# Performance work log

Hardware: AMD Instinct MI355X
Metric: run time of the kernel (lower is better)

Reference implementation:

```python
import jax, jax.numpy as jnp
from jax import lax
import numpy as np

P_NUM = 63
CHANNEL = 64
KSIZE = 5
PAD = KSIZE // 2
MEAN = jnp.linspace(-310.0, 310.0, P_NUM).reshape(1, 1, P_NUM, 1, 1)
DN = ('NCHW', 'OIHW', 'NCHW')


def rep_pad(x, p=PAD):
    return jnp.pad(x, ((0, 0), (0, 0), (p, p), (p, p)), mode='edge')


def conv(x, w, b):
    out = lax.conv_general_dilated(x, w, (1, 1), 'VALID', dimension_numbers=DN)
    return out + b[None, :, None, None]


def conv_transpose(x, w):
    # torch conv_transpose2d with weight (in, out, k, k), stride 1, no pad ==
    # full correlation with spatially flipped, in/out-transposed kernel
    k = jnp.flip(w, (-2, -1)).transpose(1, 0, 2, 3)  # (out, in, k, k)
    kh = KSIZE - 1
    return lax.conv_general_dilated(x, k, (1, 1), [(kh, kh), (kh, kh)], dimension_numbers=DN)


def crop(x, p=PAD):
    return x[:, :, p:-p, p:-p]


def act(x, w, gradient=False):
    # x: (B,C,H,W); w: (1,C,P,1,1); Gaussian-mixture RBF activation
    d = x[:, :, None, :, :] - MEAN                 # (B,C,P,H,W)
    g = jnp.exp(d * d / -200.0)
    if gradient:
        g = g * (d / -100.0)
    return (g * w).sum(axis=2)                     # (B,C,H,W)


def setup_inputs() -> dict:
    key = jax.random.key(0)
    ks = jax.random.split(key, 8)
    B, H, W = 4, 128, 128
    return {
        'x': jax.random.uniform(ks[0], (B, 1, H, W), jnp.float32),
        'y': jax.random.uniform(ks[1], (B, 1, H, W), jnp.float32),
        'lam': 0,
        'f0': jax.random.normal(ks[2], (CHANNEL, 1, KSIZE, KSIZE), jnp.float32) * 0.1,
        'b0': jax.random.normal(ks[3], (CHANNEL,), jnp.float32) * 0.01,
        'f1': jax.random.normal(ks[4], (1, CHANNEL, KSIZE, KSIZE), jnp.float32) * 0.1,
        'b1': jax.random.normal(ks[5], (1,), jnp.float32) * 0.01,
        'w0': jax.random.normal(ks[6], (1, CHANNEL, P_NUM, 1, 1), jnp.float32) * 0.1,
        'w1': jax.random.normal(ks[7], (1, 1, P_NUM, 1, 1), jnp.float32) * 0.1,
        'lam_param': jnp.float32(np.log(0.1)),
    }


def reference(x, y, lam, f0, b0, f1, b1, w0, w1, lam_param):
    del lam  # third forward arg is ignored by the original module
    x = x * 255.0
    y = y * 255.0
    xx = x
    # encoder
    c0 = conv(rep_pad(x), f0, b0)        # (B,C,H,W)
    a0 = act(c0, w0)
    c1 = conv(rep_pad(a0), f1, b1)       # (B,1,H,W)
    a1 = act(c1, w1)
    # decoder (gradient-like path)
    d = crop(conv_transpose(a1, f1))     # (B,C,H,W)
    d = d * act(c0, w0, gradient=True)
    d = crop(conv_transpose(d, f0))      # (B,1,H,W)
    out = (xx - (d + jnp.exp(lam_param) * (xx - y))) / 255.0
    return out
```

## Files before the change

kernel.cpp:

```cpp
#include <hip/hip_runtime.h>
#include <hip/hip_bf16.h>

#define BSZ 4
#define CH 64
#define IH 128
#define IW 128
#define PN 63
#define TLS 32
#define TLH 36
#define XSD 40
#define NT 64
#define CG 4
#define NG 16
#define NPOS 324
#define NPIX (BSZ*IH*IW)
#define BT 384
#define TBN 142
#define TBH 5.0f
#define TBLO (-355.0f)

__global__ __launch_bounds__(160) void kT(const float* __restrict__ w0,
                                          const float* __restrict__ w1,
                                          float4* __restrict__ tab) {
    __shared__ float wsh[PN];
    const int ch = blockIdx.x;
    const float* w = (ch < CH) ? (w0 + (size_t)ch * PN) : w1;
    if (threadIdx.x < PN) wsh[threadIdx.x] = w[threadIdx.x];
    __syncthreads();
    const int i = threadIdx.x;
    if (i >= TBN) return;
    const float x0 = TBLO + TBH * i, xm = x0 + 0.5f * TBH, x1 = x0 + TBH;
    float f0 = 0.f, fm = 0.f, f1 = 0.f;
    for (int p = 0; p < PN; ++p) {
        const float mu = -310.0f + 10.0f * (float)p, wv = wsh[p];
        const float d0 = x0 - mu, dm = xm - mu, d1 = x1 - mu;
        f0 = __fmaf_rn(wv, __expf(d0 * d0 * -0.005f), f0);
        fm = __fmaf_rn(wv, __expf(dm * dm * -0.005f), fm);
        f1 = __fmaf_rn(wv, __expf(d1 * d1 * -0.005f), f1);
    }
    tab[(size_t)ch * TBN + i] =
        make_float4(f0, -3.f * f0 + 4.f * fm - f1, 2.f * f0 - 4.f * fm + 2.f * f1, 0.f);
}

__device__ __forceinline__ void act_tab4(const float* __restrict__ v,
                                         const float4* __restrict__ tb,
                                         float* __restrict__ av,
                                         float* __restrict__ ag) {
    float t[4];
    int idx[4];
#pragma unroll
    for (int k = 0; k < 4; ++k) {
        float u = __fmaf_rn(v[k], 1.0f / TBH, -TBLO / TBH);
        u = fminf(fmaxf(u, 0.0f), (float)TBN);
        idx[k] = min((int)u, TBN - 1);
        t[k] = u - (float)idx[k];
    }
    float4 c[4];
#pragma unroll
    for (int k = 0; k < 4; ++k) c[k] = tb[idx[k]];
#pragma unroll
    for (int k = 0; k < 4; ++k) {
        av[k] = __fmaf_rn(t[k], __fmaf_rn(t[k], c[k].z, c[k].y), c[k].x);
        ag[k] = __fmaf_rn(t[k] + t[k], c[k].z, c[k].y) * (1.0f / TBH);
    }
}

__device__ __forceinline__ float act_tab_v(float v, const float4* __restrict__ tb) {
    float u = __fmaf_rn(v, 1.0f / TBH, -TBLO / TBH);
    u = fminf(fmaxf(u, 0.0f), (float)TBN);
    const int idx = min((int)u, TBN - 1);
    const float t = u - (float)idx;
    const float4 c = tb[idx];
    return __fmaf_rn(t, __fmaf_rn(t, c.z, c.y), c.x);
}

__global__ __launch_bounds__(BT) void kAB(const float* __restrict__ x,
                                          const float* __restrict__ f0,
                                          const float* __restrict__ b0,
                                          const float* __restrict__ f1,
                                          const float4* __restrict__ tab,
                                          float* __restrict__ c1p,
                                          __hip_bfloat16* __restrict__ g0out) {
    __shared__ float xs[XSD * XSD];
    __shared__ float a0s[CG][TLH * TLH];
    __shared__ float4 tbs[CG][TBN];

    const int tile = blockIdx.x;
    const int cgi  = blockIdx.y;
    const int cg   = cgi * CG;
    const int b    = tile >> 4;
    const int t    = tile & 15;
    const int h0   = (t >> 2) * TLS;
    const int w0p  = (t & 3) * TLS;
    const int tid  = threadIdx.x;

    for (int i = tid; i < XSD * XSD; i += BT) {
        int iy = i / XSD, ix = i - iy * XSD;
        int gy = min(max(h0 + iy - 4, 0), IH - 1);
        int gx = min(max(w0p + ix - 4, 0), IW - 1);
        xs[i] = x[((size_t)b * IH + gy) * IW + gx] * 255.0f;
    }
    for (int i = tid; i < CG * TBN; i += BT) {
        int cc = i / TBN, k = i - cc * TBN;
        tbs[cc][k] = tab[(size_t)(cg + cc) * TBN + k];
    }
    __syncthreads();

    if (tid < NPOS) {
        const int p = tid;
        const int pyb = p / 18, pxb = p - pyb * 18;
        const int py = 2 * pyb, px = 2 * pxb;
        float win[6][6];
#pragma unroll
        for (int r = 0; r < 6; ++r) {
            const float2* rp = (const float2*)&xs[(py + r) * XSD + px];
            float2 p0 = rp[0], p1 = rp[1], p2 = rp[2];
            win[r][0] = p0.x; win[r][1] = p0.y; win[r][2] = p1.x;
            win[r][3] = p1.y; win[r][4] = p2.x; win[r][5] = p2.y;
        }
        const bool vint = (py >= 2) && (py < 34) && (px >= 2) && (px < 34);
        const int gy0 = h0 + py - 2, gx0 = w0p + px - 2;

#pragma unroll
        for (int cc = 0; cc < CG; ++cc) {
            const int c = cg + cc;
            const float bias = b0[c];
            float acc[4] = {bias, bias, bias, bias};
#pragma unroll
            for (int u = 0; u < 5; ++u)
#pragma unroll
                for (int v = 0; v < 5; ++v) {
                    const float kv = f0[(size_t)c * 25 + u * 5 + v];
                    acc[0] = __fmaf_rn(win[u][v],         kv, acc[0]);
                    acc[1] = __fmaf_rn(win[u][v + 1],     kv, acc[1]);
                    acc[2] = __fmaf_rn(win[u + 1][v],     kv, acc[2]);
                    acc[3] = __fmaf_rn(win[u + 1][v + 1], kv, acc[3]);
                }
            float av[4], ag[4];
            act_tab4(acc, tbs[cc], av, ag);
            *(float2*)&a0s[cc][py * TLH + px]       = make_float2(av[0], av[1]);
            *(float2*)&a0s[cc][(py + 1) * TLH + px] = make_float2(av[2], av[3]);
            if (vint) {
                const size_t gb = ((size_t)b * CH + c) * (IH * IW);
                __hip_bfloat162 r0 = {__float2bfloat16(ag[0]), __float2bfloat16(ag[1])};
                __hip_bfloat162 r1 = {__float2bfloat16(ag[2]), __float2bfloat16(ag[3])};
                *(__hip_bfloat162*)&g0out[gb + (size_t)gy0 * IW + gx0]       = r0;
                *(__hip_bfloat162*)&g0out[gb + (size_t)(gy0 + 1) * IW + gx0] = r1;
            }
        }
    }
    __syncthreads();

    if (h0 == 0 || h0 == IH - TLS || w0p == 0 || w0p == IW - TLS) {
        for (int p = tid; p < TLH * TLH; p += BT) {
            const int py = p / TLH, px = p - py * TLH;
            const int gy = h0 + py - 2, gx = w0p + px - 2;
            if ((unsigned)gy >= IH || (unsigned)gx >= IW) {
                const int cpy = min(max(gy, 0), IH - 1) - h0 + 2;
                const int cpx = min(max(gx, 0), IW - 1) - w0p + 2;
                const int src = cpy * TLH + cpx;
#pragma unroll
                for (int cc = 0; cc < CG; ++cc)
                    a0s[cc][p] = a0s[cc][src];
            }
        }
    }
    __syncthreads();

    if (tid < 256) {
        const int lx = tid & 15, ly = tid >> 4;
        const int r0 = 2 * ly, c0 = 2 * lx;
        float a00 = 0.f, a01 = 0.f, a10 = 0.f, a11 = 0.f;

#pragma unroll
        for (int cc = 0; cc < CG; ++cc) {
            float win[6][6];
#pragma unroll
            for (int r = 0; r < 6; ++r) {
                const float2* rp = (const float2*)&a0s[cc][(r0 + r) * TLH + c0];
                float2 p0 = rp[0], p1 = rp[1], p2 = rp[2];
                win[r][0] = p0.x; win[r][1] = p0.y; win[r][2] = p1.x;
                win[r][3] = p1.y; win[r][4] = p2.x; win[r][5] = p2.y;
            }
#pragma unroll
            for (int u = 0; u < 5; ++u)
#pragma unroll
                for (int v = 0; v < 5; ++v) {
                    const float kv = f1[(size_t)(cg + cc) * 25 + u * 5 + v];
                    a00 = __fmaf_rn(win[u][v],         kv, a00);
                    a01 = __fmaf_rn(win[u][v + 1],     kv, a01);
                    a10 = __fmaf_rn(win[u + 1][v],     kv, a10);
                    a11 = __fmaf_rn(win[u + 1][v + 1], kv, a11);
                }
        }

        const size_t base = (size_t)cgi * NPIX + ((size_t)b * IH + h0 + r0) * IW + w0p + c0;
        *(float2*)&c1p[base]      = make_float2(a00, a01);
        *(float2*)&c1p[base + IW] = make_float2(a10, a11);
    }
}

__global__ __launch_bounds__(256) void kB2(const float* __restrict__ c1p,
                                           const float* __restrict__ b1,
                                           const float4* __restrict__ tab,
                                           float* __restrict__ a1) {
    __shared__ float4 tbs[TBN];
    const int tid = threadIdx.x;
    if (tid < TBN) tbs[tid] = tab[(size_t)CH * TBN + tid];
    __syncthreads();

    const int pid = blockIdx.x * 256 + tid;
    float vv = b1[0];
#pragma unroll
    for (int g = 0; g < NG; ++g) vv += c1p[(size_t)g * NPIX + pid];
    a1[pid] = act_tab_v(vv, tbs);
}

__global__ __launch_bounds__(BT) void kCD(const float* __restrict__ a1,
                                          const float* __restrict__ f1,
                                          const float* __restrict__ f0,
                                          const __hip_bfloat16* __restrict__ g0,
                                          float* __restrict__ d3p) {
    __shared__ float a1s[XSD * XSD];
    __shared__ float dbs[CG][TLH * TLH];

    const int tile = blockIdx.x;
    const int cgi  = blockIdx.y;
    const int cg   = cgi * CG;
    const int b    = tile >> 4;
    const int t    = tile & 15;
    const int h0   = (t >> 2) * TLS;
    const int w0p  = (t & 3) * TLS;
    const int tid  = threadIdx.x;

    for (int p = tid; p < XSD * XSD; p += BT) {
        int iy = p / XSD, ix = p - iy * XSD;
        int gy = h0 + iy - 4, gx = w0p + ix - 4;
        float v = 0.0f;
        if ((unsigned)gy < IH && (unsigned)gx < IW)
            v = a1[((size_t)b * IH + gy) * IW + gx];
        a1s[p] = v;
    }
    __syncthreads();

    if (tid < NPOS) {
        const int p = tid;
        const int pyb = p / 18, pxb = p - pyb * 18;
        const int py = 2 * pyb, px = 2 * pxb;
        const int gy0 = h0 + py - 2, gx0 = w0p + px - 2;
        const bool inb = ((unsigned)gy0 < IH) && ((unsigned)gx0 < IW);

        __hip_bfloat162 gr0[CG], gr1[CG];
#pragma unroll
        for (int cc = 0; cc < CG; ++cc) {
            __hip_bfloat162 z; z.x = __float2bfloat16(0.f); z.y = z.x;
            gr0[cc] = z; gr1[cc] = z;
            if (inb) {
                const size_t gb = ((size_t)b * CH + cg + cc) * (IH * IW);
                gr0[cc] = *(const __hip_bfloat162*)&g0[gb + (size_t)gy0 * IW + gx0];
                gr1[cc] = *(const __hip_bfloat162*)&g0[gb + (size_t)(gy0 + 1) * IW + gx0];
            }
        }

        float win[6][6];
#pragma unroll
        for (int r = 0; r < 6; ++r) {
            const float2* rp = (const float2*)&a1s[(py + r) * XSD + px];
            float2 p0 = rp[0], p1 = rp[1], p2 = rp[2];
            win[r][0] = p0.x; win[r][1] = p0.y; win[r][2] = p1.x;
            win[r][3] = p1.y; win[r][4] = p2.x; win[r][5] = p2.y;
        }

#pragma unroll
        for (int cc = 0; cc < CG; ++cc) {
            const int c = cg + cc;
            float d00 = 0.f, d01 = 0.f, d10 = 0.f, d11 = 0.f;
#pragma unroll
            for (int u = 0; u < 5; ++u)
#pragma unroll
                for (int v = 0; v < 5; ++v) {
                    const float kv = f1[(size_t)c * 25 + u * 5 + v];
                    d00 = __fmaf_rn(win[4 - u][4 - v], kv, d00);
                    d01 = __fmaf_rn(win[4 - u][5 - v], kv, d01);
                    d10 = __fmaf_rn(win[5 - u][4 - v], kv, d10);
                    d11 = __fmaf_rn(win[5 - u][5 - v], kv, d11);
                }
            const float o00 = d00 * __bfloat162float(gr0[cc].x);
            const float o01 = d01 * __bfloat162float(gr0[cc].y);
            const float o10 = d10 * __bfloat162float(gr1[cc].x);
            const float o11 = d11 * __bfloat162float(gr1[cc].y);
            *(float2*)&dbs[cc][py * TLH + px]       = make_float2(o00, o01);
            *(float2*)&dbs[cc][(py + 1) * TLH + px] = make_float2(o10, o11);
        }
    }
    __syncthreads();

    if (tid < 256) {
        const int lx = tid & 15, ly = tid >> 4;
        const int r0 = 2 * ly, c0 = 2 * lx;
        float a00 = 0.f, a01 = 0.f, a10 = 0.f, a11 = 0.f;

#pragma unroll
        for (int cc = 0; cc < CG; ++cc) {
            float win[6][6];
#pragma unroll
            for (int r = 0; r < 6; ++r) {
                const float2* rp = (const float2*)&dbs[cc][(r0 + r) * TLH + c0];
                float2 p0 = rp[0], p1 = rp[1], p2 = rp[2];
                win[r][0] = p0.x; win[r][1] = p0.y; win[r][2] = p1.x;
                win[r][3] = p1.y; win[r][4] = p2.x; win[r][5] = p2.y;
            }
#pragma unroll
            for (int u = 0; u < 5; ++u)
#pragma unroll
                for (int v = 0; v < 5; ++v) {
                    const float kv = f0[(size_t)(cg + cc) * 25 + u * 5 + v];
                    a00 = __fmaf_rn(win[4 - u][4 - v], kv, a00);
                    a01 = __fmaf_rn(win[4 - u][5 - v], kv, a01);
                    a10 = __fmaf_rn(win[5 - u][4 - v], kv, a10);
                    a11 = __fmaf_rn(win[5 - u][5 - v], kv, a11);
                }
        }

        const size_t base = (size_t)cgi * NPIX + ((size_t)b * IH + h0 + r0) * IW + w0p + c0;
        *(float2*)&d3p[base]      = make_float2(a00, a01);
        *(float2*)&d3p[base + IW] = make_float2(a10, a11);
    }
}

__global__ __launch_bounds__(256) void kE(const float* __restrict__ d3p,
                                          const float* __restrict__ x,
                                          const float* __restrict__ y,
                                          const float* __restrict__ lam_param,
                                          float* __restrict__ out) {
    const int pid = blockIdx.x * 256 + threadIdx.x;
    float d3 = 0.0f;
#pragma unroll
    for (int g = 0; g < NG; ++g) d3 += d3p[(size_t)g * NPIX + pid];
    const float elam = __expf(lam_param[0]);
    const float xv = x[pid], yv = y[pid];
    out[pid] = xv - d3 * (1.0f / 255.0f) - elam * (xv - yv);
}

extern "C" void kernel_launch(void* const* d_in, const int* in_sizes, int n_in,
                              void* d_out, int out_size, void* d_ws, size_t ws_size,
                              hipStream_t stream) {
    const float* x   = (const float*)d_in[0];
    const float* y   = (const float*)d_in[1];
    const float* f0  = (const float*)d_in[3];
    const float* b0  = (const float*)d_in[4];
    const float* f1  = (const float*)d_in[5];
    const float* b1  = (const float*)d_in[6];
    const float* w0  = (const float*)d_in[7];
    const float* w1  = (const float*)d_in[8];
    const float* lam = (const float*)d_in[9];
    float* out = (float*)d_out;

    const size_t nch = (size_t)BSZ * CH * IH * IW;
    __hip_bfloat16* g0 = (__hip_bfloat16*)d_ws;
    float4* tab = (float4*)(g0 + nch);
    float* c1p  = (float*)(tab + (size_t)(CH + 1) * TBN);
    float* a1   = c1p + (size_t)NG * NPIX;
    float* d3p  = a1 + NPIX;

    kT <<<CH + 1, 160, 0, stream>>>(w0, w1, tab);
    kAB<<<dim3(NT, NG), BT, 0, stream>>>(x, f0, b0, f1, tab, c1p, g0);
    kB2<<<NPIX / 256, 256, 0, stream>>>(c1p, b1, tab, a1);
    kCD<<<dim3(NT, NG), BT, 0, stream>>>(a1, f1, f0, g0, d3p);
    kE <<<NPIX / 256, 256, 0, stream>>>(d3p, x, y, lam, out);
}
```

Baseline: 121.5 us.

## Fuse c1 partial reduction into kCD and store partials as bf16

Removes the kB2 kernel: kCD now sums the 16 channel-group partials of c1 for its halo tile and applies the w1 activation table on the fly. The c1 and d3 partial buffers are stored in bf16 instead of fp32, halving their write and read traffic. In exchange, each kCD block redoes the 16-way reduction and table lookup for its overlapping halo (and all 16 channel-group blocks repeat it), and bf16 partials lose precision in values scaled by 255.

```diff
diff --git a/kernel.cpp b/kernel.cpp
--- a/kernel.cpp
+++ b/kernel.cpp
@@ -65,7 +65,7 @@
     }
 }
 
-__device__ __forceinline__ float act_tab_v(float v, const float4* __restrict__ tb) {
+__device__ __forceinline__ float act_tab_g(float v, const float4* __restrict__ tb) {
     float u = __fmaf_rn(v, 1.0f / TBH, -TBLO / TBH);
     u = fminf(fmaxf(u, 0.0f), (float)TBN);
     const int idx = min((int)u, TBN - 1);
@@ -79,7 +79,7 @@
                                           const float* __restrict__ b0,
                                           const float* __restrict__ f1,
                                           const float4* __restrict__ tab,
-                                          float* __restrict__ c1p,
+                                          __hip_bfloat16* __restrict__ c1p,
                                           __hip_bfloat16* __restrict__ g0out) {
     __shared__ float xs[XSD * XSD];
     __shared__ float a0s[CG][TLH * TLH];
@@ -195,32 +195,20 @@
         }
 
         const size_t base = (size_t)cgi * NPIX + ((size_t)b * IH + h0 + r0) * IW + w0p + c0;
-        *(float2*)&c1p[base]      = make_float2(a00, a01);
-        *(float2*)&c1p[base + IW] = make_float2(a10, a11);
-    }
-}
-
-__global__ __launch_bounds__(256) void kB2(const float* __restrict__ c1p,
-                                           const float* __restrict__ b1,
-                                           const float4* __restrict__ tab,
-                                           float* __restrict__ a1) {
-    __shared__ float4 tbs[TBN];
-    const int tid = threadIdx.x;
-    if (tid < TBN) tbs[tid] = tab[(size_t)CH * TBN + tid];
-    __syncthreads();
-
-    const int pid = blockIdx.x * 256 + tid;
-    float vv = b1[0];
-#pragma unroll
-    for (int g = 0; g < NG; ++g) vv += c1p[(size_t)g * NPIX + pid];
-    a1[pid] = act_tab_v(vv, tbs);
-}
-
-__global__ __launch_bounds__(BT) void kCD(const float* __restrict__ a1,
+        __hip_bfloat162 q0 = {__float2bfloat16(a00), __float2bfloat16(a01)};
+        __hip_bfloat162 q1 = {__float2bfloat16(a10), __float2bfloat16(a11)};
+        *(__hip_bfloat162*)&c1p[base]      = q0;
+        *(__hip_bfloat162*)&c1p[base + IW] = q1;
+    }
+}
+
+__global__ __launch_bounds__(BT) void kCD(const __hip_bfloat16* __restrict__ c1p,
+                                          const float* __restrict__ b1,
+                                          const float4* __restrict__ tab,
                                           const float* __restrict__ f1,
                                           const float* __restrict__ f0,
                                           const __hip_bfloat16* __restrict__ g0,
-                                          float* __restrict__ d3p) {
+                                          __hip_bfloat16* __restrict__ d3p) {
     __shared__ float a1s[XSD * XSD];
     __shared__ float dbs[CG][TLH * TLH];
 
@@ -233,12 +221,21 @@
     const int w0p  = (t & 3) * TLS;
     const int tid  = threadIdx.x;
 
+    const float b1v = b1[0];
+    const float4* tabW1 = tab + (size_t)CH * TBN;
+
     for (int p = tid; p < XSD * XSD; p += BT) {
         int iy = p / XSD, ix = p - iy * XSD;
         int gy = h0 + iy - 4, gx = w0p + ix - 4;
         float v = 0.0f;
-        if ((unsigned)gy < IH && (unsigned)gx < IW)
-            v = a1[((size_t)b * IH + gy) * IW + gx];
+        if ((unsigned)gy < IH && (unsigned)gx < IW) {
+            const size_t pix = ((size_t)b * IH + gy) * IW + gx;
+            float s = b1v;
+#pragma unroll
+            for (int g = 0; g < NG; ++g)
+                s += __bfloat162float(c1p[(size_t)g * NPIX + pix]);
+            v = act_tab_g(s, tabW1);
+        }
         a1s[p] = v;
     }
     __syncthreads();
@@ -323,12 +320,14 @@
         }
 
         const size_t base = (size_t)cgi * NPIX + ((size_t)b * IH + h0 + r0) * IW + w0p + c0;
-        *(float2*)&d3p[base]      = make_float2(a00, a01);
-        *(float2*)&d3p[base + IW] = make_float2(a10, a11);
-    }
-}
-
-__global__ __launch_bounds__(256) void kE(const float* __restrict__ d3p,
+        __hip_bfloat162 q0 = {__float2bfloat16(a00), __float2bfloat16(a01)};
+        __hip_bfloat162 q1 = {__float2bfloat16(a10), __float2bfloat16(a11)};
+        *(__hip_bfloat162*)&d3p[base]      = q0;
+        *(__hip_bfloat162*)&d3p[base + IW] = q1;
+    }
+}
+
+__global__ __launch_bounds__(256) void kE(const __hip_bfloat16* __restrict__ d3p,
                                           const float* __restrict__ x,
                                           const float* __restrict__ y,
                                           const float* __restrict__ lam_param,
@@ -336,7 +335,8 @@
     const int pid = blockIdx.x * 256 + threadIdx.x;
     float d3 = 0.0f;
 #pragma unroll
-    for (int g = 0; g < NG; ++g) d3 += d3p[(size_t)g * NPIX + pid];
+    for (int g = 0; g < NG; ++g)
+        d3 += __bfloat162float(d3p[(size_t)g * NPIX + pid]);
     const float elam = __expf(lam_param[0]);
     const float xv = x[pid], yv = y[pid];
     out[pid] = xv - d3 * (1.0f / 255.0f) - elam * (xv - yv);
@@ -359,13 +359,11 @@
     const size_t nch = (size_t)BSZ * CH * IH * IW;
     __hip_bfloat16* g0 = (__hip_bfloat16*)d_ws;
     float4* tab = (float4*)(g0 + nch);
-    float* c1p  = (float*)(tab + (size_t)(CH + 1) * TBN);
-    float* a1   = c1p + (size_t)NG * NPIX;
-    float* d3p  = a1 + NPIX;
+    __hip_bfloat16* c1p = (__hip_bfloat16*)(tab + (size_t)(CH + 1) * TBN);
+    __hip_bfloat16* d3p = c1p + (size_t)NG * NPIX;
 
     kT <<<CH + 1, 160, 0, stream>>>(w0, w1, tab);
     kAB<<<dim3(NT, NG), BT, 0, stream>>>(x, f0, b0, f1, tab, c1p, g0);
-    kB2<<<NPIX / 256, 256, 0, stream>>>(c1p, b1, tab, a1);
-    kCD<<<dim3(NT, NG), BT, 0, stream>>>(a1, f1, f0, g0, d3p);
+    kCD<<<dim3(NT, NG), BT, 0, stream>>>(c1p, b1, tab, f1, f0, g0, d3p);
     kE <<<NPIX / 256, 256, 0, stream>>>(d3p, x, y, lam, out);
 }
```

Result: no change. 122.9 us (+1.1%).
